# Kernel tuning notes

Measured on AMD Instinct MI355X. Metric: run time of the kernel, lower is better.

The kernel has to match this reference:

```python
import jax, jax.numpy as jnp
import numpy as np

N_NODES = 50000
N_EDGES = 800000
HIDDEN = 128
BN_EPS = 1e-5
LEAKY_SLOPE = 0.01


def setup_inputs() -> dict:
    key = jax.random.key(0)
    ks = jax.random.split(key, 8)
    x = jax.random.normal(ks[0], (N_NODES, HIDDEN), dtype=jnp.float32)
    edge_index = jax.random.randint(ks[1], (2, N_EDGES), 0, N_NODES, dtype=jnp.int64)
    # stacked per-layer params (4 SAGEConv layers, all 128->128)
    sc = 1.0 / np.sqrt(HIDDEN)
    Wl = jax.random.normal(ks[2], (4, HIDDEN, HIDDEN), dtype=jnp.float32) * sc
    bl = jax.random.normal(ks[3], (4, HIDDEN), dtype=jnp.float32) * sc
    Wr = jax.random.normal(ks[4], (4, HIDDEN, HIDDEN), dtype=jnp.float32) * sc
    gamma = jnp.ones((4, HIDDEN), dtype=jnp.float32)
    beta = jnp.zeros((4, HIDDEN), dtype=jnp.float32)
    return {"x": x, "edge_index": edge_index, "Wl": Wl, "bl": bl,
            "Wr": Wr, "gamma": gamma, "beta": beta}


def _sage_mean_agg(x, src, dst, n):
    # gather source features per edge, scatter-mean onto destination nodes
    msg = x[src]                                                  # [E, F]
    agg = jax.ops.segment_sum(msg, dst, num_segments=n)           # [N, F]
    cnt = jax.ops.segment_sum(jnp.ones_like(dst, dtype=x.dtype), dst, num_segments=n)
    return agg / jnp.maximum(cnt, 1.0)[:, None]


def _bn_train(x, g, b):
    mu = jnp.mean(x, axis=0)
    var = jnp.mean((x - mu) ** 2, axis=0)  # biased variance (PyTorch BN normalization)
    return (x - mu) * jax.lax.rsqrt(var + BN_EPS) * g + b


def reference(x, edge_index, Wl, bl, Wr, gamma, beta):
    src, dst = edge_index[0], edge_index[1]
    n = x.shape[0]
    h = x
    for i in range(4):
        agg = _sage_mean_agg(h, src, dst, n)
        h = agg @ Wl[i] + bl[i] + h @ Wr[i]          # SAGEConv: lin_l(mean_nbr) + lin_r(root)
        h = jnp.where(h >= 0, h, LEAKY_SLOPE * h)    # leaky_relu
        h = _bn_train(h, gamma[i], beta[i])
    # dropout: eval-mode identity (deterministic reference)
    return h
```

## Files before the change

kernel.cpp:

```cpp
#include <hip/hip_runtime.h>
#include <hip/hip_bf16.h>

#define N_NODES 50000
#define N_EDGES 800000
#define F 128
#define BN_EPS 1e-5f
#define SLOPE 0.01f
#define NB 782
#define CAP 64
#define NBIN 128
#define BINSZ 391
#define QCAP2 8192
#define ABLK 512
#define AITER 7

typedef __attribute__((ext_vector_type(8))) __bf16 bf16x8_t;
typedef __attribute__((ext_vector_type(8))) unsigned short u16x8_t;
typedef __attribute__((ext_vector_type(4))) float f32x4_t;

__device__ __forceinline__ unsigned short f2b(float f) {
    unsigned int u = __float_as_uint(f);
    unsigned int r = (u + 0x7fffu + ((u >> 16) & 1u)) >> 16;
    return (unsigned short)r;
}
__device__ __forceinline__ float b2f_lo(unsigned int v) { return __uint_as_float(v << 16); }
__device__ __forceinline__ float b2f_hi(unsigned int v) { return __uint_as_float(v & 0xffff0000u); }

__global__ __launch_bounds__(256) void bucket2_kernel(const int* __restrict__ src,
                                                      const int* __restrict__ dst,
                                                      int* __restrict__ qtail,
                                                      unsigned int* __restrict__ qdata) {
    __shared__ int counts[NBIN];
    __shared__ int cur[NBIN];
    __shared__ int base[NBIN];
    const int tid = threadIdx.x;

    for (int k = tid; k < NBIN; k += 256) { counts[k] = 0; cur[k] = 0; }
    __syncthreads();

    unsigned int pack[AITER];
    int bin[AITER];
    const int stride = ABLK * 256;
#pragma unroll
    for (int it = 0; it < AITER; ++it) {
        const int e = blockIdx.x * 256 + tid + it * stride;
        bin[it] = -1;
        if (e < N_EDGES) {
            int d = __builtin_nontemporal_load(dst + e);
            int s = __builtin_nontemporal_load(src + e);
            bin[it] = d / BINSZ;
            pack[it] = ((unsigned int)d << 16) | (unsigned int)s;
            atomicAdd(&counts[bin[it]], 1);
        }
    }
    __syncthreads();
    if (tid < NBIN) {
        int c = counts[tid];
        base[tid] = (c > 0) ? atomicAdd(&qtail[tid * 16], c) : 0;
    }
    __syncthreads();
#pragma unroll
    for (int it = 0; it < AITER; ++it) {
        if (bin[it] >= 0) {
            int slot = base[bin[it]] + atomicAdd(&cur[bin[it]], 1);
            qdata[(long)bin[it] * QCAP2 + slot] = pack[it];
        }
    }
}

__global__ __launch_bounds__(256) void scatter2_kernel(const unsigned int* __restrict__ qdata,
                                                       const int* __restrict__ qtail,
                                                       int* __restrict__ deg,
                                                       unsigned short* __restrict__ csr) {
    __shared__ int cnt[BINSZ];
    __shared__ unsigned short stage[BINSZ][CAP];
    const int b = blockIdx.x;
    const int nbase = b * BINSZ;
    const int nn = min(BINSZ, N_NODES - nbase);
    const int tid = threadIdx.x;

    for (int r = tid; r < BINSZ; r += 256) cnt[r] = 0;
    __syncthreads();

    const int n = qtail[b * 16];
    const unsigned int* q = qdata + (long)b * QCAP2;
    for (int i = tid; i < n; i += 256) {
        unsigned int p = q[i];
        int local = (int)(p >> 16) - nbase;
        int pos = atomicAdd(&cnt[local], 1);
        if (pos < CAP) stage[local][pos] = (unsigned short)(p & 0xffff);
    }
    __syncthreads();

    for (int c = tid; c < nn * (CAP / 8); c += 256) {
        const int r = c >> 3;
        const int col = (c & 7) * 8;
        *(u16x8_t*)(csr + (long)(nbase + r) * CAP + col) = *(const u16x8_t*)&stage[r][col];
    }
    for (int r = tid; r < nn; r += 256) deg[nbase + r] = min(cnt[r], CAP);
}


__global__ __launch_bounds__(256) void f2b_kernel(const float* __restrict__ in,
                                                  unsigned short* __restrict__ out) {
    long i = (long)blockIdx.x * blockDim.x + threadIdx.x;
    if (i >= (long)N_NODES * (F / 4)) return;
    float4 v = ((const float4*)in)[i];
    ushort4 o;
    o.x = f2b(v.x); o.y = f2b(v.y); o.z = f2b(v.z); o.w = f2b(v.w);
    ((ushort4*)out)[i] = o;
}

__global__ __launch_bounds__(256) void wprep_kernel(const float* __restrict__ Wl,
                                                    const float* __restrict__ Wr,
                                                    unsigned short* __restrict__ Wt) {
    int idx = blockIdx.x * blockDim.x + threadIdx.x;
    if (idx >= 4 * F * 256) return;
    int k = idx & 255;
    int n = (idx >> 8) & 127;
    int i = idx >> 15;
    float v = (k < F) ? Wl[((long)i * F + k) * F + n] : Wr[((long)i * F + (k - F)) * F + n];
    Wt[idx] = f2b(v);
}

__global__ void ident_kernel(float* __restrict__ scale, float* __restrict__ shift) {
    int j = threadIdx.x;
    if (j < F) { scale[j] = 1.f; shift[j] = 0.f; }
}


__global__ __launch_bounds__(256) void agg_kernel(const unsigned short* __restrict__ h,
                                                  const int* __restrict__ deg,
                                                  const unsigned short* __restrict__ csr,
                                                  const float* __restrict__ scale,
                                                  const float* __restrict__ shift,
                                                  unsigned short* __restrict__ agg) {
    int node = (int)((blockIdx.x * (unsigned)blockDim.x + threadIdx.x) >> 6);
    int lane = threadIdx.x & 63;
    if (node >= N_NODES) return;
    const int d = deg[node];
    const int beg = node * CAP;
    const int end = beg + d;
    const unsigned short* hl = h + lane * 2;
    float ax = 0.f, ay = 0.f;
    for (int e = beg; e < end; e += 16) {
        int idx[16];
#pragma unroll
        for (int j = 0; j < 16; ++j) {
            int ee = e + j;
            idx[j] = (int)csr[(ee < end) ? ee : beg];
        }
        unsigned int v[16];
#pragma unroll
        for (int j = 0; j < 16; ++j)
            v[j] = *(const unsigned int*)(hl + (long)idx[j] * F);
#pragma unroll
        for (int j = 0; j < 16; ++j) {
            unsigned int m = (e + j < end) ? v[j] : 0u;
            ax += b2f_lo(m);
            ay += b2f_hi(m);
        }
    }
    if (d > 0) {
        const float inv = 1.0f / (float)d;
        const float2 sc = ((const float2*)scale)[lane];
        const float2 sh = ((const float2*)shift)[lane];
        ax = ax * inv * sc.x + sh.x;
        ay = ay * inv * sc.y + sh.y;
    } else {
        ax = 0.f; ay = 0.f;
    }
    unsigned int o = (unsigned int)f2b(ax) | ((unsigned int)f2b(ay) << 16);
    *(unsigned int*)(agg + (long)node * F + lane * 2) = o;
}

__device__ __forceinline__ u16x8_t affine8(u16x8_t av, const float* __restrict__ sc,
                                           const float* __restrict__ sh) {
    u16x8_t r;
#pragma unroll
    for (int j = 0; j < 8; ++j) {
        float v = __uint_as_float(((unsigned int)av[j]) << 16);
        v = v * sc[j] + sh[j];
        r[j] = f2b(v);
    }
    return r;
}

__global__ __launch_bounds__(256) void gemm_mfma(const unsigned short* __restrict__ aggb,
                                                 const unsigned short* __restrict__ hin,
                                                 const float* __restrict__ scale,
                                                 const float* __restrict__ shift,
                                                 const unsigned short* __restrict__ Wt,
                                                 const float* __restrict__ bl,
                                                 float* __restrict__ Pf,
                                                 unsigned short* __restrict__ Pb,
                                                 int write_bf16,
                                                 float* __restrict__ partial) {
    __shared__ __align__(16) char shraw[64 * 136 * 4];
    unsigned short* stage = (unsigned short*)shraw;
    unsigned short* ep16 = (unsigned short*)shraw;
    float* ep32 = (float*)shraw;
    __shared__ float lsum[4][F];
    __shared__ float lsq[4][F];

    const int tid = threadIdx.x;
    const int wave = tid >> 6, lane = tid & 63;
    const int m = lane & 15, q = lane >> 4;
    const int rbase = blockIdx.x * 64 + wave * 16;
    const int arow = rbase + m;
    const bool aval = arow < N_NODES;
    const unsigned short* ap = aggb + (long)arow * F + q * 8;
    const unsigned short* hp = hin + (long)arow * F + q * 8;

    u16x8_t areg[8];
#pragma unroll
    for (int j = 0; j < 8; ++j) areg[j] = (u16x8_t)0;
    if (aval) {
#pragma unroll
        for (int j = 0; j < 4; ++j) areg[j] = *(const u16x8_t*)(ap + j * 32);
#pragma unroll
        for (int j = 0; j < 4; ++j) {
            u16x8_t raw = *(const u16x8_t*)(hp + j * 32);
            const int base = j * 32 + q * 8;
            areg[4 + j] = affine8(raw, scale + base, shift + base);
        }
    }

    f32x4_t acc[8];
#pragma unroll
    for (int nt = 0; nt < 8; ++nt) acc[nt] = (f32x4_t){0.f, 0.f, 0.f, 0.f};

    for (int half = 0; half < 2; ++half) {
        if (half) __syncthreads();
#pragma unroll
        for (int f = 0; f < 8; ++f) {
            const int fid = f * 256 + tid;
            const int lf = fid & 63;
            const int ksf = (fid >> 6) & 3;
            const int ntf = fid >> 8;
            const int n = ntf * 16 + (lf & 15);
            const int k = half * 128 + ksf * 32 + (lf >> 4) * 8;
            *(u16x8_t*)(stage + fid * 8) = *(const u16x8_t*)(Wt + (long)n * 256 + k);
        }
        __syncthreads();
#pragma unroll
        for (int ks = 0; ks < 4; ++ks) {
            bf16x8_t af = __builtin_bit_cast(bf16x8_t, areg[half * 4 + ks]);
#pragma unroll
            for (int nt = 0; nt < 8; ++nt) {
                u16x8_t bv = *(const u16x8_t*)(stage + ((nt * 4 + ks) * 64 + lane) * 8);
                bf16x8_t bf = __builtin_bit_cast(bf16x8_t, bv);
                acc[nt] = __builtin_amdgcn_mfma_f32_16x16x32_bf16(af, bf, acc[nt], 0, 0, 0);
            }
        }
    }

    __syncthreads();

    float cs[8], cq[8];
#pragma unroll
    for (int nt = 0; nt < 8; ++nt) {
        cs[nt] = 0.f; cq[nt] = 0.f;
        const int c = nt * 16 + m;
        const float b = bl[c];
#pragma unroll
        for (int r = 0; r < 4; ++r) {
            const int rl = wave * 16 + q * 4 + r;
            float v = acc[nt][r] + b;
            v = (v >= 0.f) ? v : SLOPE * v;
            if (write_bf16) ep16[rl * 136 + c] = f2b(v);
            else            ep32[rl * 136 + c] = v;
            if (rbase + q * 4 + r < N_NODES) {
                cs[nt] += v;
                cq[nt] += v * v;
            }
        }
    }

    {
        const int rq = lane >> 4;
        const int cc = (lane & 15) * 8;
#pragma unroll
        for (int r2 = 0; r2 < 4; ++r2) {
            const int rl = wave * 16 + rq * 4 + r2;
            const int grow = blockIdx.x * 64 + rl;
            if (grow < N_NODES) {
                if (write_bf16) {
                    *(u16x8_t*)(Pb + (long)grow * F + cc) =
                        *(const u16x8_t*)(ep16 + rl * 136 + cc);
                } else {
                    *(f32x4_t*)(Pf + (long)grow * F + cc) =
                        *(const f32x4_t*)(ep32 + rl * 136 + cc);
                    *(f32x4_t*)(Pf + (long)grow * F + cc + 4) =
                        *(const f32x4_t*)(ep32 + rl * 136 + cc + 4);
                }
            }
        }
    }

#pragma unroll
    for (int nt = 0; nt < 8; ++nt) {
        cs[nt] += __shfl_xor(cs[nt], 16);
        cs[nt] += __shfl_xor(cs[nt], 32);
        cq[nt] += __shfl_xor(cq[nt], 16);
        cq[nt] += __shfl_xor(cq[nt], 32);
    }
    if (lane < 16) {
#pragma unroll
        for (int nt = 0; nt < 8; ++nt) {
            lsum[wave][nt * 16 + m] = cs[nt];
            lsq[wave][nt * 16 + m] = cq[nt];
        }
    }
    __syncthreads();
    if (tid < F) {
        float s = 0.f, s2 = 0.f;
#pragma unroll
        for (int w = 0; w < 4; ++w) {
            s += lsum[w][tid];
            s2 += lsq[w][tid];
        }
        partial[(long)blockIdx.x * 256 + tid] = s;
        partial[(long)blockIdx.x * 256 + 128 + tid] = s2;
    }
}

__global__ __launch_bounds__(256) void bn_reduce(const float* __restrict__ partial,
                                                 const float* __restrict__ gamma,
                                                 const float* __restrict__ beta,
                                                 float* __restrict__ scale,
                                                 float* __restrict__ shift) {
    const int j = blockIdx.x;
    const int t = threadIdx.x;
    const int lane = t & 63, wave = t >> 6;
    float s = 0.f, s2 = 0.f;
    for (int b = t; b < NB; b += 256) {
        s += partial[(long)b * 256 + j];
        s2 += partial[(long)b * 256 + 128 + j];
    }
#pragma unroll
    for (int off = 1; off < 64; off <<= 1) {
        s += __shfl_xor(s, off);
        s2 += __shfl_xor(s2, off);
    }
    __shared__ float ls[4], lq[4];
    if (lane == 0) { ls[wave] = s; lq[wave] = s2; }
    __syncthreads();
    if (t == 0) {
        float S = ls[0] + ls[1] + ls[2] + ls[3];
        float Q = lq[0] + lq[1] + lq[2] + lq[3];
        const float inv_n = 1.0f / (float)N_NODES;
        float mu = S * inv_n;
        float var = Q * inv_n - mu * mu;
        float scl = gamma[j] * rsqrtf(var + BN_EPS);
        scale[j] = scl;
        shift[j] = beta[j] - mu * scl;
    }
}

__global__ __launch_bounds__(256) void bn_apply_f(float* __restrict__ P,
                                                  const float* __restrict__ scale,
                                                  const float* __restrict__ shift) {
    long i = (long)blockIdx.x * blockDim.x + threadIdx.x;
    if (i >= (long)N_NODES * (F / 4)) return;
    const int c4 = (int)(i & 31);
    float4 v = ((float4*)P)[i];
    const float4 sc = ((const float4*)scale)[c4];
    const float4 sh = ((const float4*)shift)[c4];
    v.x = v.x * sc.x + sh.x;
    v.y = v.y * sc.y + sh.y;
    v.z = v.z * sc.z + sh.z;
    v.w = v.w * sc.w + sh.w;
    ((float4*)P)[i] = v;
}


extern "C" void kernel_launch(void* const* d_in, const int* in_sizes, int n_in,
                              void* d_out, int out_size, void* d_ws, size_t ws_size,
                              hipStream_t stream) {
    const float* x     = (const float*)d_in[0];
    const int*   ei    = (const int*)d_in[1];
    const float* Wl    = (const float*)d_in[2];
    const float* bl    = (const float*)d_in[3];
    const float* Wr    = (const float*)d_in[4];
    const float* gamma = (const float*)d_in[5];
    const float* beta  = (const float*)d_in[6];
    float* out = (float*)d_out;

    const int* src = ei;
    const int* dst = ei + N_EDGES;

    char* w = (char*)d_ws;
    auto alloc = [&](size_t bytes) -> char* {
        char* p = w;
        w += (bytes + 255) & ~(size_t)255;
        return p;
    };
    unsigned short* hbA   = (unsigned short*)alloc((size_t)N_NODES * F * 2);
    unsigned short* hbB   = (unsigned short*)alloc((size_t)N_NODES * F * 2);
    unsigned short* aggb  = (unsigned short*)alloc((size_t)N_NODES * F * 2);
    unsigned short* Wt    = (unsigned short*)alloc((size_t)4 * F * 256 * 2);
    int*   deg      = (int*)alloc((size_t)N_NODES * 4);
    int*   qtail    = (int*)alloc((size_t)NBIN * 16 * 4);
    unsigned int* qdata = (unsigned int*)alloc((size_t)NBIN * QCAP2 * 4);
    unsigned short* csr = (unsigned short*)alloc((size_t)N_NODES * CAP * 2);
    float* partial  = (float*)alloc((size_t)NB * 256 * 4);
    float* scale    = (float*)alloc(F * 4);
    float* shift    = (float*)alloc(F * 4);

    hipMemsetAsync(qtail, 0, (size_t)NBIN * 16 * 4, stream);

    bucket2_kernel<<<ABLK, 256, 0, stream>>>(src, dst, qtail, qdata);
    scatter2_kernel<<<NBIN, 256, 0, stream>>>(qdata, qtail, deg, csr);

    const int n4 = N_NODES * (F / 4);
    f2b_kernel<<<(n4 + 255) / 256, 256, 0, stream>>>(x, hbA);
    wprep_kernel<<<(4 * F * 256 + 255) / 256, 256, 0, stream>>>(Wl, Wr, Wt);
    ident_kernel<<<1, 128, 0, stream>>>(scale, shift);

    unsigned short* hin = hbA;
    unsigned short* hnext = hbB;
    for (int i = 0; i < 4; ++i) {
        const int last = (i == 3);

        agg_kernel<<<(N_NODES + 3) / 4, 256, 0, stream>>>(hin, deg, csr, scale, shift, aggb);

        gemm_mfma<<<NB, 256, 0, stream>>>(
            aggb, hin, scale, shift, Wt + (size_t)i * F * 256, bl + (size_t)i * F,
            out, hnext, last ? 0 : 1, partial);

        bn_reduce<<<F, 256, 0, stream>>>(partial, gamma + (size_t)i * F, beta + (size_t)i * F,
                                         scale, shift);

        unsigned short* t = hin; hin = hnext; hnext = t;
    }
    bn_apply_f<<<(n4 + 255) / 256, 256, 0, stream>>>(out, scale, shift);
}
```

Before: 368.5 us.

## Aggregate two nodes per wave, halve GEMM row tile, keep final layer bf16

The aggregation kernel now has each wave process two destination nodes at once, interleaving their neighbor gathers to expose more memory-level parallelism. The GEMM tile drops from 64 to 32 rows per block, with wave pairs splitting the output columns, which doubles the block count and shrinks shared memory. The last layer now writes bf16 like the others, and the final BN apply reads bf16 and expands to fp32. That removes the fp32 epilogue path but adds a bf16 rounding step before the final normalization. Work in the two-node wave is bounded by the larger degree, so lanes idle when the two degrees differ.

```diff
diff --git a/kernel.cpp b/kernel.cpp
--- a/kernel.cpp
+++ b/kernel.cpp
@@ -6,7 +6,7 @@
 #define F 128
 #define BN_EPS 1e-5f
 #define SLOPE 0.01f
-#define NB 782
+#define NB 1563
 #define CAP 64
 #define NBIN 128
 #define BINSZ 391
@@ -25,6 +25,7 @@
 }
 __device__ __forceinline__ float b2f_lo(unsigned int v) { return __uint_as_float(v << 16); }
 __device__ __forceinline__ float b2f_hi(unsigned int v) { return __uint_as_float(v & 0xffff0000u); }
+
 
 __global__ __launch_bounds__(256) void bucket2_kernel(const int* __restrict__ src,
                                                       const int* __restrict__ dst,
@@ -135,43 +136,59 @@
                                                   const float* __restrict__ scale,
                                                   const float* __restrict__ shift,
                                                   unsigned short* __restrict__ agg) {
-    int node = (int)((blockIdx.x * (unsigned)blockDim.x + threadIdx.x) >> 6);
-    int lane = threadIdx.x & 63;
-    if (node >= N_NODES) return;
-    const int d = deg[node];
-    const int beg = node * CAP;
-    const int end = beg + d;
+    const int wid = (int)((blockIdx.x * (unsigned)blockDim.x + threadIdx.x) >> 6);
+    const int lane = threadIdx.x & 63;
+    const int n0 = wid * 2;
+    const int n1 = n0 + 1;
+    if (n0 >= N_NODES) return;
+    const bool has1 = n1 < N_NODES;
+    const int d0 = deg[n0];
+    const int d1 = has1 ? deg[n1] : 0;
+    const int b0 = n0 * CAP, b1 = n1 * CAP;
     const unsigned short* hl = h + lane * 2;
-    float ax = 0.f, ay = 0.f;
-    for (int e = beg; e < end; e += 16) {
-        int idx[16];
+    float ax0 = 0.f, ay0 = 0.f, ax1 = 0.f, ay1 = 0.f;
+    const int dm = (d0 > d1) ? d0 : d1;
+    for (int off = 0; off < dm; off += 16) {
+        int i0[16], i1[16];
 #pragma unroll
         for (int j = 0; j < 16; ++j) {
-            int ee = e + j;
-            idx[j] = (int)csr[(ee < end) ? ee : beg];
-        }
-        unsigned int v[16];
-#pragma unroll
-        for (int j = 0; j < 16; ++j)
-            v[j] = *(const unsigned int*)(hl + (long)idx[j] * F);
+            const int e = off + j;
+            i0[j] = (int)csr[b0 + ((e < d0) ? e : 0)];
+            i1[j] = has1 ? (int)csr[b1 + ((e < d1) ? e : 0)] : i0[j];
+        }
+        unsigned int v0[16], v1[16];
 #pragma unroll
         for (int j = 0; j < 16; ++j) {
-            unsigned int m = (e + j < end) ? v[j] : 0u;
-            ax += b2f_lo(m);
-            ay += b2f_hi(m);
-        }
-    }
-    if (d > 0) {
-        const float inv = 1.0f / (float)d;
-        const float2 sc = ((const float2*)scale)[lane];
-        const float2 sh = ((const float2*)shift)[lane];
-        ax = ax * inv * sc.x + sh.x;
-        ay = ay * inv * sc.y + sh.y;
-    } else {
-        ax = 0.f; ay = 0.f;
-    }
-    unsigned int o = (unsigned int)f2b(ax) | ((unsigned int)f2b(ay) << 16);
-    *(unsigned int*)(agg + (long)node * F + lane * 2) = o;
+            v0[j] = *(const unsigned int*)(hl + (long)i0[j] * F);
+            v1[j] = *(const unsigned int*)(hl + (long)i1[j] * F);
+        }
+#pragma unroll
+        for (int j = 0; j < 16; ++j) {
+            const int e = off + j;
+            unsigned int m0 = (e < d0) ? v0[j] : 0u;
+            unsigned int m1 = (e < d1) ? v1[j] : 0u;
+            ax0 += b2f_lo(m0); ay0 += b2f_hi(m0);
+            ax1 += b2f_lo(m1); ay1 += b2f_hi(m1);
+        }
+    }
+    const float2 sc = ((const float2*)scale)[lane];
+    const float2 sh = ((const float2*)shift)[lane];
+    if (d0 > 0) {
+        const float inv = 1.0f / (float)d0;
+        ax0 = ax0 * inv * sc.x + sh.x;
+        ay0 = ay0 * inv * sc.y + sh.y;
+    } else { ax0 = 0.f; ay0 = 0.f; }
+    *(unsigned int*)(agg + (long)n0 * F + lane * 2) =
+        (unsigned int)f2b(ax0) | ((unsigned int)f2b(ay0) << 16);
+    if (has1) {
+        if (d1 > 0) {
+            const float inv = 1.0f / (float)d1;
+            ax1 = ax1 * inv * sc.x + sh.x;
+            ay1 = ay1 * inv * sc.y + sh.y;
+        } else { ax1 = 0.f; ay1 = 0.f; }
+        *(unsigned int*)(agg + (long)n1 * F + lane * 2) =
+            (unsigned int)f2b(ax1) | ((unsigned int)f2b(ay1) << 16);
+    }
 }
 
 __device__ __forceinline__ u16x8_t affine8(u16x8_t av, const float* __restrict__ sc,
@@ -192,21 +209,20 @@
                                                  const float* __restrict__ shift,
                                                  const unsigned short* __restrict__ Wt,
                                                  const float* __restrict__ bl,
-                                                 float* __restrict__ Pf,
                                                  unsigned short* __restrict__ Pb,
-                                                 int write_bf16,
                                                  float* __restrict__ partial) {
-    __shared__ __align__(16) char shraw[64 * 136 * 4];
+    __shared__ __align__(16) char shraw[16384];
     unsigned short* stage = (unsigned short*)shraw;
     unsigned short* ep16 = (unsigned short*)shraw;
-    float* ep32 = (float*)shraw;
-    __shared__ float lsum[4][F];
-    __shared__ float lsq[4][F];
+    __shared__ float lsum[4][64];
+    __shared__ float lsq[4][64];
 
     const int tid = threadIdx.x;
     const int wave = tid >> 6, lane = tid & 63;
+    const int p = wave & 1;
+    const int wr = wave >> 1;
     const int m = lane & 15, q = lane >> 4;
-    const int rbase = blockIdx.x * 64 + wave * 16;
+    const int rbase = blockIdx.x * 32 + wr * 16;
     const int arow = rbase + m;
     const bool aval = arow < N_NODES;
     const unsigned short* ap = aggb + (long)arow * F + q * 8;
@@ -226,29 +242,31 @@
         }
     }
 
-    f32x4_t acc[8];
-#pragma unroll
-    for (int nt = 0; nt < 8; ++nt) acc[nt] = (f32x4_t){0.f, 0.f, 0.f, 0.f};
-
-    for (int half = 0; half < 2; ++half) {
-        if (half) __syncthreads();
-#pragma unroll
-        for (int f = 0; f < 8; ++f) {
+    f32x4_t acc[4];
+#pragma unroll
+    for (int nt = 0; nt < 4; ++nt) acc[nt] = (f32x4_t){0.f, 0.f, 0.f, 0.f};
+
+#pragma unroll
+    for (int qtr = 0; qtr < 4; ++qtr) {
+        if (qtr) __syncthreads();
+#pragma unroll
+        for (int f = 0; f < 4; ++f) {
             const int fid = f * 256 + tid;
             const int lf = fid & 63;
-            const int ksf = (fid >> 6) & 3;
-            const int ntf = fid >> 8;
+            const int ksl = (fid >> 6) & 1;
+            const int ntf = fid >> 7;
             const int n = ntf * 16 + (lf & 15);
-            const int k = half * 128 + ksf * 32 + (lf >> 4) * 8;
+            const int k = (qtr * 2 + ksl) * 32 + (lf >> 4) * 8;
             *(u16x8_t*)(stage + fid * 8) = *(const u16x8_t*)(Wt + (long)n * 256 + k);
         }
         __syncthreads();
 #pragma unroll
-        for (int ks = 0; ks < 4; ++ks) {
-            bf16x8_t af = __builtin_bit_cast(bf16x8_t, areg[half * 4 + ks]);
-#pragma unroll
-            for (int nt = 0; nt < 8; ++nt) {
-                u16x8_t bv = *(const u16x8_t*)(stage + ((nt * 4 + ks) * 64 + lane) * 8);
+        for (int ksl = 0; ksl < 2; ++ksl) {
+            bf16x8_t af = __builtin_bit_cast(bf16x8_t, areg[qtr * 2 + ksl]);
+#pragma unroll
+            for (int nt = 0; nt < 4; ++nt) {
+                const int gnt = p * 4 + nt;
+                u16x8_t bv = *(const u16x8_t*)(stage + ((gnt * 2 + ksl) * 64 + lane) * 8);
                 bf16x8_t bf = __builtin_bit_cast(bf16x8_t, bv);
                 acc[nt] = __builtin_amdgcn_mfma_f32_16x16x32_bf16(af, bf, acc[nt], 0, 0, 0);
             }
@@ -257,49 +275,26 @@
 
     __syncthreads();
 
-    float cs[8], cq[8];
-#pragma unroll
-    for (int nt = 0; nt < 8; ++nt) {
+    float cs[4], cq[4];
+#pragma unroll
+    for (int nt = 0; nt < 4; ++nt) {
         cs[nt] = 0.f; cq[nt] = 0.f;
-        const int c = nt * 16 + m;
-        const float b = bl[c];
+        const int cg = p * 64 + nt * 16 + m;
+        const float b = bl[cg];
 #pragma unroll
         for (int r = 0; r < 4; ++r) {
-            const int rl = wave * 16 + q * 4 + r;
+            const int rl = wr * 16 + q * 4 + r;
             float v = acc[nt][r] + b;
             v = (v >= 0.f) ? v : SLOPE * v;
-            if (write_bf16) ep16[rl * 136 + c] = f2b(v);
-            else            ep32[rl * 136 + c] = v;
+            ep16[rl * 136 + cg] = f2b(v);
             if (rbase + q * 4 + r < N_NODES) {
                 cs[nt] += v;
                 cq[nt] += v * v;
             }
         }
     }
-
-    {
-        const int rq = lane >> 4;
-        const int cc = (lane & 15) * 8;
-#pragma unroll
-        for (int r2 = 0; r2 < 4; ++r2) {
-            const int rl = wave * 16 + rq * 4 + r2;
-            const int grow = blockIdx.x * 64 + rl;
-            if (grow < N_NODES) {
-                if (write_bf16) {
-                    *(u16x8_t*)(Pb + (long)grow * F + cc) =
-                        *(const u16x8_t*)(ep16 + rl * 136 + cc);
-                } else {
-                    *(f32x4_t*)(Pf + (long)grow * F + cc) =
-                        *(const f32x4_t*)(ep32 + rl * 136 + cc);
-                    *(f32x4_t*)(Pf + (long)grow * F + cc + 4) =
-                        *(const f32x4_t*)(ep32 + rl * 136 + cc + 4);
-                }
-            }
-        }
-    }
-
-#pragma unroll
-    for (int nt = 0; nt < 8; ++nt) {
+#pragma unroll
+    for (int nt = 0; nt < 4; ++nt) {
         cs[nt] += __shfl_xor(cs[nt], 16);
         cs[nt] += __shfl_xor(cs[nt], 32);
         cq[nt] += __shfl_xor(cq[nt], 16);
@@ -307,21 +302,25 @@
     }
     if (lane < 16) {
 #pragma unroll
-        for (int nt = 0; nt < 8; ++nt) {
+        for (int nt = 0; nt < 4; ++nt) {
             lsum[wave][nt * 16 + m] = cs[nt];
             lsq[wave][nt * 16 + m] = cq[nt];
         }
     }
     __syncthreads();
+
+    for (int c = tid; c < 32 * 16; c += 256) {
+        const int r = c >> 4;
+        const int col = (c & 15) * 8;
+        const int grow = blockIdx.x * 32 + r;
+        if (grow < N_NODES)
+            *(u16x8_t*)(Pb + (long)grow * F + col) = *(const u16x8_t*)(ep16 + r * 136 + col);
+    }
+
     if (tid < F) {
-        float s = 0.f, s2 = 0.f;
-#pragma unroll
-        for (int w = 0; w < 4; ++w) {
-            s += lsum[w][tid];
-            s2 += lsq[w][tid];
-        }
-        partial[(long)blockIdx.x * 256 + tid] = s;
-        partial[(long)blockIdx.x * 256 + 128 + tid] = s2;
+        const int ph = tid >> 6, cl = tid & 63;
+        partial[(long)blockIdx.x * 256 + tid] = lsum[ph][cl] + lsum[ph + 2][cl];
+        partial[(long)blockIdx.x * 256 + 128 + tid] = lsq[ph][cl] + lsq[ph + 2][cl];
     }
 }
 
@@ -358,20 +357,29 @@
     }
 }
 
-__global__ __launch_bounds__(256) void bn_apply_f(float* __restrict__ P,
+__global__ __launch_bounds__(256) void bn_apply_f(const unsigned short* __restrict__ Pb,
+                                                  float* __restrict__ out,
                                                   const float* __restrict__ scale,
                                                   const float* __restrict__ shift) {
     long i = (long)blockIdx.x * blockDim.x + threadIdx.x;
-    if (i >= (long)N_NODES * (F / 4)) return;
-    const int c4 = (int)(i & 31);
-    float4 v = ((float4*)P)[i];
-    const float4 sc = ((const float4*)scale)[c4];
-    const float4 sh = ((const float4*)shift)[c4];
-    v.x = v.x * sc.x + sh.x;
-    v.y = v.y * sc.y + sh.y;
-    v.z = v.z * sc.z + sh.z;
-    v.w = v.w * sc.w + sh.w;
-    ((float4*)P)[i] = v;
+    if (i >= (long)N_NODES * (F / 8)) return;
+    const int c8 = (int)(i & 15);
+    uint4 v = ((const uint4*)Pb)[i];
+    const float4 sc0 = ((const float4*)scale)[c8 * 2];
+    const float4 sc1 = ((const float4*)scale)[c8 * 2 + 1];
+    const float4 sh0 = ((const float4*)shift)[c8 * 2];
+    const float4 sh1 = ((const float4*)shift)[c8 * 2 + 1];
+    float4 o0, o1;
+    o0.x = b2f_lo(v.x) * sc0.x + sh0.x;
+    o0.y = b2f_hi(v.x) * sc0.y + sh0.y;
+    o0.z = b2f_lo(v.y) * sc0.z + sh0.z;
+    o0.w = b2f_hi(v.y) * sc0.w + sh0.w;
+    o1.x = b2f_lo(v.z) * sc1.x + sh1.x;
+    o1.y = b2f_hi(v.z) * sc1.y + sh1.y;
+    o1.z = b2f_lo(v.w) * sc1.z + sh1.z;
+    o1.w = b2f_hi(v.w) * sc1.w + sh1.w;
+    ((float4*)out)[i * 2] = o0;
+    ((float4*)out)[i * 2 + 1] = o1;
 }
 
 
@@ -414,6 +422,7 @@
     scatter2_kernel<<<NBIN, 256, 0, stream>>>(qdata, qtail, deg, csr);
 
     const int n4 = N_NODES * (F / 4);
+    const int n8 = N_NODES * (F / 8);
     f2b_kernel<<<(n4 + 255) / 256, 256, 0, stream>>>(x, hbA);
     wprep_kernel<<<(4 * F * 256 + 255) / 256, 256, 0, stream>>>(Wl, Wr, Wt);
     ident_kernel<<<1, 128, 0, stream>>>(scale, shift);
@@ -421,18 +430,17 @@
     unsigned short* hin = hbA;
     unsigned short* hnext = hbB;
     for (int i = 0; i < 4; ++i) {
-        const int last = (i == 3);
-
-        agg_kernel<<<(N_NODES + 3) / 4, 256, 0, stream>>>(hin, deg, csr, scale, shift, aggb);
+        agg_kernel<<<(N_NODES / 2 + 3) / 4, 256, 0, stream>>>(hin, deg, csr, scale, shift,
+                                                              aggb);
 
         gemm_mfma<<<NB, 256, 0, stream>>>(
             aggb, hin, scale, shift, Wt + (size_t)i * F * 256, bl + (size_t)i * F,
-            out, hnext, last ? 0 : 1, partial);
+            hnext, partial);
 
         bn_reduce<<<F, 256, 0, stream>>>(partial, gamma + (size_t)i * F, beta + (size_t)i * F,
                                          scale, shift);
 
         unsigned short* t = hin; hin = hnext; hnext = t;
     }
-    bn_apply_f<<<(n4 + 255) / 256, 256, 0, stream>>>(out, scale, shift);
-}
+    bn_apply_f<<<(n8 + 255) / 256, 256, 0, stream>>>(hin, out, scale, shift);
+}
```

Result: slower. 391.4 us (+6.2%).
